# Optimization experiments

Hardware: AMD Instinct MI355X
Metric: run time of the kernel (lower is better)

The kernel has to match this reference:

```python
import jax, jax.numpy as jnp
import numpy as np

B, N, CQ, CH, H = 2, 2048, 256, 256, 8
D = CH // H  # head_dim = 32


def setup_inputs() -> dict:
    key = jax.random.key(0)
    ks = jax.random.split(key, 10)
    s = 0.02
    return {
        "q_x": jax.random.normal(ks[0], (B, N, CQ), dtype=jnp.float32),
        "attn_bias": jax.random.normal(ks[1], (B, H, N, N), dtype=jnp.float32),
        "Wq": jax.random.normal(ks[2], (CQ, CH), dtype=jnp.float32) * s,
        "bq": jnp.zeros((CH,), dtype=jnp.float32),
        "Wk": jax.random.normal(ks[3], (CQ, CH), dtype=jnp.float32) * s,
        "Wv": jax.random.normal(ks[4], (CQ, CH), dtype=jnp.float32) * s,
        "Wout": jax.random.normal(ks[5], (CH, CQ), dtype=jnp.float32) * s,
        "bout": jnp.zeros((CQ,), dtype=jnp.float32),
        "Wg": jax.random.normal(ks[6], (CQ, CQ), dtype=jnp.float32) * s,
        "bg": jnp.zeros((CQ,), dtype=jnp.float32),
        "gbias": jnp.ones((CQ,), dtype=jnp.float32),
    }


def reference(q_x, attn_bias, Wq, bq, Wk, Wv, Wout, bout, Wg, bg, gbias):
    # prep_qkv: project, split heads; scale q by 1/sqrt(head_dim) (apply_scale path)
    scale = 1.0 / jnp.sqrt(jnp.asarray(D, q_x.dtype))
    q = ((q_x @ Wq + bq).reshape(B, N, H, D)) * scale  # [B,N,H,D]
    k = (q_x @ Wk).reshape(B, N, H, D)
    v = (q_x @ Wv).reshape(B, N, H, D)
    # attention with additive pair bias
    scores = jnp.einsum("bqhd,bkhd->bhqk", q, k) + attn_bias  # [B,H,N,N]
    attn = jax.nn.softmax(scores, axis=-1)
    o = jnp.einsum("bhqk,bkhd->bqhd", attn, v).reshape(B, N, CH)  # merge heads
    # wrap_up: output projection + sigmoid gate (gating_bias init ones)
    out = o @ Wout + bout  # [B,N,CQ]
    gate = jax.nn.sigmoid(q_x @ Wg + bg + gbias)
    return gate * out
```

## Files before the change

### kernel.cpp

```cpp
#include <hip/hip_runtime.h>

typedef __bf16 bf16_t;
typedef bf16_t bf16x8 __attribute__((ext_vector_type(8)));
typedef float f32x4 __attribute__((ext_vector_type(4)));
typedef unsigned short ushort8 __attribute__((ext_vector_type(8)));

#define LOG2E 1.4426950408889634f

static __device__ __forceinline__ unsigned short f2bf(float f) {
  union { float f; unsigned u; } a; a.f = f;
  unsigned r = a.u + 0x7FFFu + ((a.u >> 16) & 1u);
  return (unsigned short)(r >> 16);
}

static __device__ __forceinline__ bf16x8 ldb8(const unsigned short* p) {
  return *reinterpret_cast<const bf16x8*>(p);
}

__global__ __launch_bounds__(256) void prep_k(
    const float* __restrict__ Wq, const float* __restrict__ Wk,
    const float* __restrict__ Wv, const float* __restrict__ Wg,
    const float* __restrict__ Wo, const float* __restrict__ X,
    unsigned short* __restrict__ wt, unsigned short* __restrict__ xb) {
  const int bid = blockIdx.x;
  if (bid < 320) {
    __shared__ float t[32][33];
    const int w = bid >> 6, tile = bid & 63;
    const int r0 = (tile >> 3) * 32, c0 = (tile & 7) * 32;
    const float* W = (w == 0) ? Wq : (w == 1) ? Wk : (w == 2) ? Wv : (w == 3) ? Wg : Wo;
    const int x = threadIdx.x & 31, y = threadIdx.x >> 5;
#pragma unroll
    for (int yy = 0; yy < 32; yy += 8) t[y + yy][x] = W[(r0 + y + yy) * 256 + c0 + x];
    __syncthreads();
#pragma unroll
    for (int yy = 0; yy < 32; yy += 8)
      wt[w * 65536 + (c0 + y + yy) * 256 + r0 + x] = f2bf(t[x][y + yy]);
  } else {
    const int i = (bid - 320) * 1024 + threadIdx.x * 4;
    const f32x4 v = *reinterpret_cast<const f32x4*>(X + i);
    unsigned short o[4];
#pragma unroll
    for (int e = 0; e < 4; ++e) o[e] = f2bf(v[e]);
    *reinterpret_cast<unsigned long long*>(xb + i) = *reinterpret_cast<unsigned long long*>(o);
  }
}

__global__ __launch_bounds__(256) void proj_k(
    const unsigned short* __restrict__ xb, const float* __restrict__ bq,
    const unsigned short* __restrict__ wt,
    unsigned short* __restrict__ q_ws, unsigned short* __restrict__ k_ws,
    unsigned short* __restrict__ vt_ws) {
  __shared__ unsigned short vtile[64][72];
  const int tid = threadIdx.x;
  const int wave = tid >> 6, l = tid & 63, g = l >> 4, l15 = l & 15;
  const int mrow = blockIdx.x * 64 + wave * 16 + l15;
  const int widx = blockIdx.y >> 2;
  const int nin0 = (blockIdx.y & 3) * 64;
  const unsigned short* W = wt + widx * 65536;

  f32x4 acc[4];
#pragma unroll
  for (int st = 0; st < 4; ++st) acc[st] = f32x4{0.f, 0.f, 0.f, 0.f};

#pragma unroll
  for (int kk0 = 0; kk0 < 256; kk0 += 32) {
    const bf16x8 av = ldb8(xb + mrow * 256 + kk0 + 8 * g);
#pragma unroll
    for (int st = 0; st < 4; ++st) {
      bf16x8 bv = ldb8(W + (nin0 + st * 16 + l15) * 256 + kk0 + 8 * g);
      acc[st] = __builtin_amdgcn_mfma_f32_16x16x32_bf16(av, bv, acc[st], 0, 0, 0);
    }
  }

  const int mb = blockIdx.x * 64 + wave * 16 + 4 * g;
  if (widx == 2) {
#pragma unroll
    for (int st = 0; st < 4; ++st)
#pragma unroll
      for (int j = 0; j < 4; ++j)
        vtile[st * 16 + l15][wave * 16 + 4 * g + j] = f2bf(acc[st][j]);
    __syncthreads();
    const int b = (blockIdx.x * 64) >> 11;
    const int t0 = (blockIdx.x * 64) & 2047;
#pragma unroll
    for (int it = tid; it < 512; it += 256) {
      const int r = it >> 3, cseg = (it & 7) * 8;
      const int n = nin0 + r;
      *reinterpret_cast<ushort8*>(vt_ws + (size_t)((b * 8 + (n >> 5)) * 32 + (n & 31)) * 2048 +
                                  t0 + cseg) = *reinterpret_cast<const ushort8*>(&vtile[r][cseg]);
    }
  } else {
#pragma unroll
    for (int st = 0; st < 4; ++st) {
      const int n = nin0 + st * 16 + l15;
      const int h = n >> 5, d = n & 31;
#pragma unroll
      for (int j = 0; j < 4; ++j) {
        const int m = mb + j;
        const int b = m >> 11, t = m & 2047;
        if (widx == 0) {
          q_ws[((b * 8 + h) * 2048 + t) * 32 + d] =
              f2bf((acc[st][j] + bq[n]) * (0.17677669529663687f * LOG2E));
        } else {
          k_ws[((b * 8 + h) * 2048 + t) * 32 + d] = f2bf(acc[st][j]);
        }
      }
    }
  }
}

__global__ __launch_bounds__(256) void attn_k(
    const unsigned short* __restrict__ q_ws, const unsigned short* __restrict__ k_ws,
    const unsigned short* __restrict__ vt_ws, const float* __restrict__ bias,
    unsigned short* __restrict__ o_ws) {
  __shared__ float sbias[4 * 3 * 1024];
  __shared__ unsigned short plds[4 * 16 * 72];
  const int tid = threadIdx.x;
  const int wave = tid >> 6, l = tid & 63, g = l >> 4, l15 = l & 15;
  const int bh = blockIdx.x >> 5, qt = blockIdx.x & 31;
  const int qr0 = qt * 64 + wave * 16;
  const int kvbase = bh * 2048;
  unsigned short* pw = plds + wave * (16 * 72);
  float* sb = sbias + wave * 3072;

  const bf16x8 qa = ldb8(q_ws + (size_t)(kvbase + qr0 + l15) * 32 + 8 * g);
  const unsigned short* kbase = k_ws + (size_t)kvbase * 32 + 8 * g + l15 * 32;
  const unsigned short* vbase = vt_ws + (size_t)(bh * 32 + l15) * 2048 + 8 * g;
  const float* bsrc = bias + ((size_t)bh << 22) + (size_t)(qr0 + (l >> 4)) * 2048 + (l & 15) * 4;

  auto stage = [&](int bidx, int k0) {
    float* dst = sb + bidx * 1024;
#pragma unroll
    for (int qq = 0; qq < 4; ++qq)
      __builtin_amdgcn_global_load_lds(
          (const __attribute__((address_space(1))) void*)(bsrc + (size_t)qq * 8192 + k0),
          (__attribute__((address_space(3))) void*)(dst + qq * 256), 16, 0, 0);
  };

  float mr[4], lr[4];
  f32x4 oacc[2];
#pragma unroll
  for (int j = 0; j < 4; ++j) { mr[j] = -1e30f; lr[j] = 0.0f; }
  oacc[0] = f32x4{0.f, 0.f, 0.f, 0.f};
  oacc[1] = f32x4{0.f, 0.f, 0.f, 0.f};

  stage(0, 0);
  stage(1, 64);
  int cb = 0;
#pragma unroll 1
  for (int kt = 0; kt < 32; ++kt) {
    const int k0 = kt * 64;
    if (kt < 31) {
      asm volatile("s_waitcnt vmcnt(4)" ::: "memory");
    } else {
      asm volatile("s_waitcnt vmcnt(0)" ::: "memory");
    }
    __builtin_amdgcn_sched_barrier(0);
    f32x4 cfr[4];
    const float* sbc = sb + cb * 1024 + l15;
#pragma unroll
    for (int st = 0; st < 4; ++st)
#pragma unroll
      for (int j = 0; j < 4; ++j)
        cfr[st][j] = sbc[(4 * g + j) * 64 + st * 16] * LOG2E;

    bf16x8 kb[4];
#pragma unroll
    for (int st = 0; st < 4; ++st) kb[st] = ldb8(kbase + (size_t)(k0 + st * 16) * 32);
    bf16x8 vb[2][2];
#pragma unroll
    for (int dst = 0; dst < 2; ++dst)
#pragma unroll
      for (int kc = 0; kc < 2; ++kc)
        vb[dst][kc] = ldb8(vbase + (size_t)dst * 16 * 2048 + k0 + kc * 32);

    int nb = cb + 2; if (nb >= 3) nb -= 3;
    if (kt < 30) stage(nb, k0 + 128);

    f32x4 s[4];
#pragma unroll
    for (int st = 0; st < 4; ++st)
      s[st] = __builtin_amdgcn_mfma_f32_16x16x32_bf16(qa, kb[st], cfr[st], 0, 0, 0);

#pragma unroll
    for (int j = 0; j < 4; ++j) {
      float mx = fmaxf(fmaxf(s[0][j], s[1][j]), fmaxf(s[2][j], s[3][j]));
      mx = fmaxf(mx, __shfl_xor(mx, 1));
      mx = fmaxf(mx, __shfl_xor(mx, 2));
      mx = fmaxf(mx, __shfl_xor(mx, 4));
      mx = fmaxf(mx, __shfl_xor(mx, 8));
      const float mn = fmaxf(mr[j], mx);
      const float sc = __builtin_amdgcn_exp2f(mr[j] - mn);
      mr[j] = mn;
      float rs = 0.f;
#pragma unroll
      for (int st = 0; st < 4; ++st) {
        float e = __builtin_amdgcn_exp2f(s[st][j] - mn);
        s[st][j] = e;
        rs += e;
      }
      rs += __shfl_xor(rs, 1);
      rs += __shfl_xor(rs, 2);
      rs += __shfl_xor(rs, 4);
      rs += __shfl_xor(rs, 8);
      lr[j] = lr[j] * sc + rs;
      oacc[0][j] *= sc;
      oacc[1][j] *= sc;
    }
#pragma unroll
    for (int st = 0; st < 4; ++st)
#pragma unroll
      for (int j = 0; j < 4; ++j)
        pw[(4 * g + j) * 72 + st * 16 + l15] = f2bf(s[st][j]);
#pragma unroll
    for (int kc = 0; kc < 2; ++kc) {
      bf16x8 pa = ldb8(pw + l15 * 72 + kc * 32 + 8 * g);
      oacc[0] = __builtin_amdgcn_mfma_f32_16x16x32_bf16(pa, vb[0][kc], oacc[0], 0, 0, 0);
      oacc[1] = __builtin_amdgcn_mfma_f32_16x16x32_bf16(pa, vb[1][kc], oacc[1], 0, 0, 0);
    }
    cb = cb + 1; if (cb >= 3) cb -= 3;
  }

  const int b = bh >> 3, h = bh & 7;
#pragma unroll
  for (int dst = 0; dst < 2; ++dst)
#pragma unroll
    for (int j = 0; j < 4; ++j) {
      const int q = qr0 + 4 * g + j;
      const float val = oacc[dst][j] / lr[j];
      o_ws[((size_t)(b * 2048 + q)) * 256 + h * 32 + dst * 16 + l15] = f2bf(val);
    }
}

__global__ __launch_bounds__(256) void outp_k(
    const unsigned short* __restrict__ o_ws, const unsigned short* __restrict__ wt,
    const unsigned short* __restrict__ xb, const float* __restrict__ bout,
    const float* __restrict__ bg, const float* __restrict__ gbias,
    float* __restrict__ out) {
  const int tid = threadIdx.x;
  const int wave = tid >> 6, l = tid & 63, g = l >> 4, l15 = l & 15;
  const int m0 = blockIdx.x * 64 + wave * 16;
  const int c0 = blockIdx.y * 64;
  const unsigned short* wgt = wt + 3 * 65536;
  const unsigned short* wot = wt + 4 * 65536;
  f32x4 acco[4], accg[4];
#pragma unroll
  for (int st = 0; st < 4; ++st) {
    acco[st] = f32x4{0.f, 0.f, 0.f, 0.f};
    accg[st] = f32x4{0.f, 0.f, 0.f, 0.f};
  }
#pragma unroll
  for (int kk0 = 0; kk0 < 256; kk0 += 32) {
    const bf16x8 a_o = ldb8(o_ws + (m0 + l15) * 256 + kk0 + 8 * g);
    const bf16x8 a_x = ldb8(xb + (m0 + l15) * 256 + kk0 + 8 * g);
#pragma unroll
    for (int st = 0; st < 4; ++st) {
      bf16x8 bo = ldb8(wot + (c0 + st * 16 + l15) * 256 + kk0 + 8 * g);
      acco[st] = __builtin_amdgcn_mfma_f32_16x16x32_bf16(a_o, bo, acco[st], 0, 0, 0);
      bf16x8 bgf = ldb8(wgt + (c0 + st * 16 + l15) * 256 + kk0 + 8 * g);
      accg[st] = __builtin_amdgcn_mfma_f32_16x16x32_bf16(a_x, bgf, accg[st], 0, 0, 0);
    }
  }
  const int mb = m0 + 4 * g;
#pragma unroll
  for (int st = 0; st < 4; ++st) {
    const int n = c0 + st * 16 + l15;
#pragma unroll
    for (int j = 0; j < 4; ++j) {
      const int m = mb + j;
      const float z = accg[st][j] + bg[n] + gbias[n];
      const float gate = 1.0f / (1.0f + __expf(-z));
      out[m * 256 + n] = gate * (acco[st][j] + bout[n]);
    }
  }
}

extern "C" void kernel_launch(void* const* d_in, const int* in_sizes, int n_in,
                              void* d_out, int out_size, void* d_ws, size_t ws_size,
                              hipStream_t stream) {
  const float* q_x   = (const float*)d_in[0];
  const float* bias  = (const float*)d_in[1];
  const float* Wq    = (const float*)d_in[2];
  const float* bq    = (const float*)d_in[3];
  const float* Wk    = (const float*)d_in[4];
  const float* Wv    = (const float*)d_in[5];
  const float* Wout  = (const float*)d_in[6];
  const float* bout  = (const float*)d_in[7];
  const float* Wg    = (const float*)d_in[8];
  const float* bg    = (const float*)d_in[9];
  const float* gbias = (const float*)d_in[10];
  float* out = (float*)d_out;

  char* ws = (char*)d_ws;
  unsigned short* wt    = (unsigned short*)(ws);
  unsigned short* xb    = (unsigned short*)(ws + 655360);
  unsigned short* q_ws  = (unsigned short*)(ws + 655360 + 2097152);
  unsigned short* k_ws  = (unsigned short*)(ws + 655360 + 2 * 2097152);
  unsigned short* vt_ws = (unsigned short*)(ws + 655360 + 3 * 2097152);
  unsigned short* o_ws  = (unsigned short*)(ws + 655360 + 4 * 2097152);

  prep_k<<<1344, 256, 0, stream>>>(Wq, Wk, Wv, Wg, Wout, q_x, wt, xb);
  proj_k<<<dim3(64, 12), 256, 0, stream>>>(xb, bq, wt, q_ws, k_ws, vt_ws);
  attn_k<<<512, 256, 0, stream>>>(q_ws, k_ws, vt_ws, bias, o_ws);
  outp_k<<<dim3(64, 4), 256, 0, stream>>>(o_ws, wt, xb, bout, bg, gbias, out);
}
```

Baseline: 112.0 us.

## Double-buffer 128-key bias tiles and issue K/V loads before bias wait

The attention kernel now stages the pair bias in 128-key tiles with two LDS buffers per wave, replacing three 64-key buffers. Each loop iteration handles two 64-key halves, which halves the number of iterations and the loop overhead. K and V fragments for both halves are loaded before the wait on the next bias tile, so their latency overlaps with it. The cost is more registers for K/V fragments, a larger LDS footprint (64KB of bias), and hand-tuned vmcnt counts that depend on the exact order of the loads.

```diff
diff --git a/kernel.cpp b/kernel.cpp
--- a/kernel.cpp
+++ b/kernel.cpp
@@ -113,28 +113,27 @@
     const unsigned short* __restrict__ q_ws, const unsigned short* __restrict__ k_ws,
     const unsigned short* __restrict__ vt_ws, const float* __restrict__ bias,
     unsigned short* __restrict__ o_ws) {
-  __shared__ float sbias[4 * 3 * 1024];
-  __shared__ unsigned short plds[4 * 16 * 72];
+  __shared__ float sbias[4][2][16][128];
+  __shared__ unsigned short plds[4][16 * 72];
   const int tid = threadIdx.x;
   const int wave = tid >> 6, l = tid & 63, g = l >> 4, l15 = l & 15;
   const int bh = blockIdx.x >> 5, qt = blockIdx.x & 31;
   const int qr0 = qt * 64 + wave * 16;
   const int kvbase = bh * 2048;
-  unsigned short* pw = plds + wave * (16 * 72);
-  float* sb = sbias + wave * 3072;
+  unsigned short* pw = plds[wave];
 
   const bf16x8 qa = ldb8(q_ws + (size_t)(kvbase + qr0 + l15) * 32 + 8 * g);
   const unsigned short* kbase = k_ws + (size_t)kvbase * 32 + 8 * g + l15 * 32;
   const unsigned short* vbase = vt_ws + (size_t)(bh * 32 + l15) * 2048 + 8 * g;
-  const float* bsrc = bias + ((size_t)bh << 22) + (size_t)(qr0 + (l >> 4)) * 2048 + (l & 15) * 4;
-
-  auto stage = [&](int bidx, int k0) {
-    float* dst = sb + bidx * 1024;
-#pragma unroll
-    for (int qq = 0; qq < 4; ++qq)
+  const float* bsrc = bias + ((size_t)bh << 22) + (size_t)(qr0 + (l >> 5)) * 2048 + (l & 31) * 4;
+
+  auto stage = [&](int buf, int kt) {
+    float* dst = &sbias[wave][buf][0][0];
+#pragma unroll
+    for (int i = 0; i < 8; ++i)
       __builtin_amdgcn_global_load_lds(
-          (const __attribute__((address_space(1))) void*)(bsrc + (size_t)qq * 8192 + k0),
-          (__attribute__((address_space(3))) void*)(dst + qq * 256), 16, 0, 0);
+          (const __attribute__((address_space(1))) void*)(bsrc + (size_t)(2 * i) * 2048 + kt * 128),
+          (__attribute__((address_space(3))) void*)(dst + i * 256), 16, 0, 0);
   };
 
   float mr[4], lr[4];
@@ -145,80 +144,81 @@
   oacc[1] = f32x4{0.f, 0.f, 0.f, 0.f};
 
   stage(0, 0);
-  stage(1, 64);
-  int cb = 0;
 #pragma unroll 1
-  for (int kt = 0; kt < 32; ++kt) {
-    const int k0 = kt * 64;
-    if (kt < 31) {
-      asm volatile("s_waitcnt vmcnt(4)" ::: "memory");
+  for (int kt = 0; kt < 16; ++kt) {
+    const int buf = kt & 1;
+    const int k0 = kt * 128;
+    bf16x8 kb[2][4];
+#pragma unroll
+    for (int h = 0; h < 2; ++h)
+#pragma unroll
+      for (int st = 0; st < 4; ++st)
+        kb[h][st] = ldb8(kbase + (size_t)(k0 + h * 64 + st * 16) * 32);
+    bf16x8 vb[2][2][2];
+#pragma unroll
+    for (int h = 0; h < 2; ++h)
+#pragma unroll
+      for (int dst = 0; dst < 2; ++dst)
+#pragma unroll
+        for (int kc = 0; kc < 2; ++kc)
+          vb[h][dst][kc] = ldb8(vbase + (size_t)dst * 16 * 2048 + k0 + h * 64 + kc * 32);
+    if (kt < 15) stage(buf ^ 1, kt + 1);
+    if (kt < 15) {
+      asm volatile("s_waitcnt vmcnt(24)" ::: "memory");
     } else {
-      asm volatile("s_waitcnt vmcnt(0)" ::: "memory");
+      asm volatile("s_waitcnt vmcnt(16)" ::: "memory");
     }
     __builtin_amdgcn_sched_barrier(0);
-    f32x4 cfr[4];
-    const float* sbc = sb + cb * 1024 + l15;
-#pragma unroll
-    for (int st = 0; st < 4; ++st)
-#pragma unroll
-      for (int j = 0; j < 4; ++j)
-        cfr[st][j] = sbc[(4 * g + j) * 64 + st * 16] * LOG2E;
-
-    bf16x8 kb[4];
-#pragma unroll
-    for (int st = 0; st < 4; ++st) kb[st] = ldb8(kbase + (size_t)(k0 + st * 16) * 32);
-    bf16x8 vb[2][2];
-#pragma unroll
-    for (int dst = 0; dst < 2; ++dst)
-#pragma unroll
-      for (int kc = 0; kc < 2; ++kc)
-        vb[dst][kc] = ldb8(vbase + (size_t)dst * 16 * 2048 + k0 + kc * 32);
-
-    int nb = cb + 2; if (nb >= 3) nb -= 3;
-    if (kt < 30) stage(nb, k0 + 128);
-
-    f32x4 s[4];
-#pragma unroll
-    for (int st = 0; st < 4; ++st)
-      s[st] = __builtin_amdgcn_mfma_f32_16x16x32_bf16(qa, kb[st], cfr[st], 0, 0, 0);
-
-#pragma unroll
-    for (int j = 0; j < 4; ++j) {
-      float mx = fmaxf(fmaxf(s[0][j], s[1][j]), fmaxf(s[2][j], s[3][j]));
-      mx = fmaxf(mx, __shfl_xor(mx, 1));
-      mx = fmaxf(mx, __shfl_xor(mx, 2));
-      mx = fmaxf(mx, __shfl_xor(mx, 4));
-      mx = fmaxf(mx, __shfl_xor(mx, 8));
-      const float mn = fmaxf(mr[j], mx);
-      const float sc = __builtin_amdgcn_exp2f(mr[j] - mn);
-      mr[j] = mn;
-      float rs = 0.f;
-#pragma unroll
-      for (int st = 0; st < 4; ++st) {
-        float e = __builtin_amdgcn_exp2f(s[st][j] - mn);
-        s[st][j] = e;
-        rs += e;
+
+#pragma unroll
+    for (int h = 0; h < 2; ++h) {
+      f32x4 cfr[4];
+#pragma unroll
+      for (int st = 0; st < 4; ++st)
+#pragma unroll
+        for (int j = 0; j < 4; ++j)
+          cfr[st][j] = sbias[wave][buf][4 * g + j][h * 64 + st * 16 + l15] * LOG2E;
+      f32x4 s[4];
+#pragma unroll
+      for (int st = 0; st < 4; ++st)
+        s[st] = __builtin_amdgcn_mfma_f32_16x16x32_bf16(qa, kb[h][st], cfr[st], 0, 0, 0);
+#pragma unroll
+      for (int j = 0; j < 4; ++j) {
+        float mx = fmaxf(fmaxf(s[0][j], s[1][j]), fmaxf(s[2][j], s[3][j]));
+        mx = fmaxf(mx, __shfl_xor(mx, 1));
+        mx = fmaxf(mx, __shfl_xor(mx, 2));
+        mx = fmaxf(mx, __shfl_xor(mx, 4));
+        mx = fmaxf(mx, __shfl_xor(mx, 8));
+        const float mn = fmaxf(mr[j], mx);
+        const float sc = __builtin_amdgcn_exp2f(mr[j] - mn);
+        mr[j] = mn;
+        float rs = 0.f;
+#pragma unroll
+        for (int st = 0; st < 4; ++st) {
+          float e = __builtin_amdgcn_exp2f(s[st][j] - mn);
+          s[st][j] = e;
+          rs += e;
+        }
+        rs += __shfl_xor(rs, 1);
+        rs += __shfl_xor(rs, 2);
+        rs += __shfl_xor(rs, 4);
+        rs += __shfl_xor(rs, 8);
+        lr[j] = lr[j] * sc + rs;
+        oacc[0][j] *= sc;
+        oacc[1][j] *= sc;
       }
-      rs += __shfl_xor(rs, 1);
-      rs += __shfl_xor(rs, 2);
-      rs += __shfl_xor(rs, 4);
-      rs += __shfl_xor(rs, 8);
-      lr[j] = lr[j] * sc + rs;
-      oacc[0][j] *= sc;
-      oacc[1][j] *= sc;
-    }
-#pragma unroll
-    for (int st = 0; st < 4; ++st)
-#pragma unroll
-      for (int j = 0; j < 4; ++j)
-        pw[(4 * g + j) * 72 + st * 16 + l15] = f2bf(s[st][j]);
-#pragma unroll
-    for (int kc = 0; kc < 2; ++kc) {
-      bf16x8 pa = ldb8(pw + l15 * 72 + kc * 32 + 8 * g);
-      oacc[0] = __builtin_amdgcn_mfma_f32_16x16x32_bf16(pa, vb[0][kc], oacc[0], 0, 0, 0);
-      oacc[1] = __builtin_amdgcn_mfma_f32_16x16x32_bf16(pa, vb[1][kc], oacc[1], 0, 0, 0);
-    }
-    cb = cb + 1; if (cb >= 3) cb -= 3;
+#pragma unroll
+      for (int st = 0; st < 4; ++st)
+#pragma unroll
+        for (int j = 0; j < 4; ++j)
+          pw[(4 * g + j) * 72 + st * 16 + l15] = f2bf(s[st][j]);
+#pragma unroll
+      for (int kc = 0; kc < 2; ++kc) {
+        bf16x8 pa = ldb8(pw + l15 * 72 + kc * 32 + 8 * g);
+        oacc[0] = __builtin_amdgcn_mfma_f32_16x16x32_bf16(pa, vb[h][0][kc], oacc[0], 0, 0, 0);
+        oacc[1] = __builtin_amdgcn_mfma_f32_16x16x32_bf16(pa, vb[h][1][kc], oacc[1], 0, 0, 0);
+      }
+    }
   }
 
   const int b = bh >> 3, h = bh & 7;
```

Measured after the change: 121.9 us. 8.9% more time.

## Fuse bf16 conversion into projection kernels and double-buffer bias staging

Applied to the files above, without the earlier changes.

Removes the separate prep kernel. The projection and output kernels now read fp32 inputs and weights directly, converting weights to bf16 and transposing them into shared memory, and converting activations to bf16 in registers. This drops one launch and a workspace round trip. In exchange, every block redoes the weight conversion, and the weight loads are strided column reads. The attention kernel also moves from triple- to double-buffered bias staging with a full vmcnt(0) wait and a launch-bounds occupancy hint, trading prefetch depth for less LDS per block.

```diff
diff --git a/kernel.cpp b/kernel.cpp
--- a/kernel.cpp
+++ b/kernel.cpp
@@ -17,46 +17,28 @@
   return *reinterpret_cast<const bf16x8*>(p);
 }
 
-__global__ __launch_bounds__(256) void prep_k(
+__global__ __launch_bounds__(256) void proj_k(
+    const float* __restrict__ X, const float* __restrict__ bq,
     const float* __restrict__ Wq, const float* __restrict__ Wk,
-    const float* __restrict__ Wv, const float* __restrict__ Wg,
-    const float* __restrict__ Wo, const float* __restrict__ X,
-    unsigned short* __restrict__ wt, unsigned short* __restrict__ xb) {
-  const int bid = blockIdx.x;
-  if (bid < 320) {
-    __shared__ float t[32][33];
-    const int w = bid >> 6, tile = bid & 63;
-    const int r0 = (tile >> 3) * 32, c0 = (tile & 7) * 32;
-    const float* W = (w == 0) ? Wq : (w == 1) ? Wk : (w == 2) ? Wv : (w == 3) ? Wg : Wo;
-    const int x = threadIdx.x & 31, y = threadIdx.x >> 5;
-#pragma unroll
-    for (int yy = 0; yy < 32; yy += 8) t[y + yy][x] = W[(r0 + y + yy) * 256 + c0 + x];
-    __syncthreads();
-#pragma unroll
-    for (int yy = 0; yy < 32; yy += 8)
-      wt[w * 65536 + (c0 + y + yy) * 256 + r0 + x] = f2bf(t[x][y + yy]);
-  } else {
-    const int i = (bid - 320) * 1024 + threadIdx.x * 4;
-    const f32x4 v = *reinterpret_cast<const f32x4*>(X + i);
-    unsigned short o[4];
-#pragma unroll
-    for (int e = 0; e < 4; ++e) o[e] = f2bf(v[e]);
-    *reinterpret_cast<unsigned long long*>(xb + i) = *reinterpret_cast<unsigned long long*>(o);
-  }
-}
-
-__global__ __launch_bounds__(256) void proj_k(
-    const unsigned short* __restrict__ xb, const float* __restrict__ bq,
-    const unsigned short* __restrict__ wt,
+    const float* __restrict__ Wv,
     unsigned short* __restrict__ q_ws, unsigned short* __restrict__ k_ws,
     unsigned short* __restrict__ vt_ws) {
+  __shared__ unsigned short wl[64][264];
   __shared__ unsigned short vtile[64][72];
   const int tid = threadIdx.x;
   const int wave = tid >> 6, l = tid & 63, g = l >> 4, l15 = l & 15;
   const int mrow = blockIdx.x * 64 + wave * 16 + l15;
   const int widx = blockIdx.y >> 2;
   const int nin0 = (blockIdx.y & 3) * 64;
-  const unsigned short* W = wt + widx * 65536;
+  const float* W = (widx == 0) ? Wq : (widx == 1) ? Wk : Wv;
+
+  {
+    const int c = tid & 63;
+#pragma unroll
+    for (int kk = tid >> 6; kk < 256; kk += 4)
+      wl[c][kk] = f2bf(W[kk * 256 + nin0 + c]);
+  }
+  __syncthreads();
 
   f32x4 acc[4];
 #pragma unroll
@@ -64,11 +46,16 @@
 
 #pragma unroll
   for (int kk0 = 0; kk0 < 256; kk0 += 32) {
-    const bf16x8 av = ldb8(xb + mrow * 256 + kk0 + 8 * g);
+    const float* xp = X + mrow * 256 + kk0 + 8 * g;
+    f32x4 x0 = *reinterpret_cast<const f32x4*>(xp);
+    f32x4 x1 = *reinterpret_cast<const f32x4*>(xp + 4);
+    union { unsigned short u[8]; bf16x8 v; } av;
+#pragma unroll
+    for (int e = 0; e < 4; ++e) { av.u[e] = f2bf(x0[e]); av.u[4 + e] = f2bf(x1[e]); }
 #pragma unroll
     for (int st = 0; st < 4; ++st) {
-      bf16x8 bv = ldb8(W + (nin0 + st * 16 + l15) * 256 + kk0 + 8 * g);
-      acc[st] = __builtin_amdgcn_mfma_f32_16x16x32_bf16(av, bv, acc[st], 0, 0, 0);
+      bf16x8 bv = ldb8(&wl[st * 16 + l15][kk0 + 8 * g]);
+      acc[st] = __builtin_amdgcn_mfma_f32_16x16x32_bf16(av.v, bv, acc[st], 0, 0, 0);
     }
   }
 
@@ -109,27 +96,26 @@
   }
 }
 
-__global__ __launch_bounds__(256) void attn_k(
+__global__ __launch_bounds__(256, 3) void attn_k(
     const unsigned short* __restrict__ q_ws, const unsigned short* __restrict__ k_ws,
     const unsigned short* __restrict__ vt_ws, const float* __restrict__ bias,
     unsigned short* __restrict__ o_ws) {
-  __shared__ float sbias[4 * 3 * 1024];
-  __shared__ unsigned short plds[4 * 16 * 72];
+  __shared__ float sbias[4][2][1024];
+  __shared__ unsigned short plds[4][16 * 72];
   const int tid = threadIdx.x;
   const int wave = tid >> 6, l = tid & 63, g = l >> 4, l15 = l & 15;
   const int bh = blockIdx.x >> 5, qt = blockIdx.x & 31;
   const int qr0 = qt * 64 + wave * 16;
   const int kvbase = bh * 2048;
-  unsigned short* pw = plds + wave * (16 * 72);
-  float* sb = sbias + wave * 3072;
+  unsigned short* pw = plds[wave];
 
   const bf16x8 qa = ldb8(q_ws + (size_t)(kvbase + qr0 + l15) * 32 + 8 * g);
   const unsigned short* kbase = k_ws + (size_t)kvbase * 32 + 8 * g + l15 * 32;
   const unsigned short* vbase = vt_ws + (size_t)(bh * 32 + l15) * 2048 + 8 * g;
   const float* bsrc = bias + ((size_t)bh << 22) + (size_t)(qr0 + (l >> 4)) * 2048 + (l & 15) * 4;
 
-  auto stage = [&](int bidx, int k0) {
-    float* dst = sb + bidx * 1024;
+  auto stage = [&](int buf, int k0) {
+    float* dst = &sbias[wave][buf][0];
 #pragma unroll
     for (int qq = 0; qq < 4; ++qq)
       __builtin_amdgcn_global_load_lds(
@@ -145,19 +131,14 @@
   oacc[1] = f32x4{0.f, 0.f, 0.f, 0.f};
 
   stage(0, 0);
-  stage(1, 64);
-  int cb = 0;
 #pragma unroll 1
   for (int kt = 0; kt < 32; ++kt) {
+    const int buf = kt & 1;
     const int k0 = kt * 64;
-    if (kt < 31) {
-      asm volatile("s_waitcnt vmcnt(4)" ::: "memory");
-    } else {
-      asm volatile("s_waitcnt vmcnt(0)" ::: "memory");
-    }
+    asm volatile("s_waitcnt vmcnt(0)" ::: "memory");
     __builtin_amdgcn_sched_barrier(0);
     f32x4 cfr[4];
-    const float* sbc = sb + cb * 1024 + l15;
+    const float* sbc = &sbias[wave][buf][0] + l15;
 #pragma unroll
     for (int st = 0; st < 4; ++st)
 #pragma unroll
@@ -174,8 +155,7 @@
       for (int kc = 0; kc < 2; ++kc)
         vb[dst][kc] = ldb8(vbase + (size_t)dst * 16 * 2048 + k0 + kc * 32);
 
-    int nb = cb + 2; if (nb >= 3) nb -= 3;
-    if (kt < 30) stage(nb, k0 + 128);
+    if (kt < 31) stage(buf ^ 1, k0 + 64);
 
     f32x4 s[4];
 #pragma unroll
@@ -218,7 +198,6 @@
       oacc[0] = __builtin_amdgcn_mfma_f32_16x16x32_bf16(pa, vb[0][kc], oacc[0], 0, 0, 0);
       oacc[1] = __builtin_amdgcn_mfma_f32_16x16x32_bf16(pa, vb[1][kc], oacc[1], 0, 0, 0);
     }
-    cb = cb + 1; if (cb >= 3) cb -= 3;
   }
 
   const int b = bh >> 3, h = bh & 7;
@@ -233,16 +212,27 @@
 }
 
 __global__ __launch_bounds__(256) void outp_k(
-    const unsigned short* __restrict__ o_ws, const unsigned short* __restrict__ wt,
-    const unsigned short* __restrict__ xb, const float* __restrict__ bout,
-    const float* __restrict__ bg, const float* __restrict__ gbias,
-    float* __restrict__ out) {
+    const unsigned short* __restrict__ o_ws, const float* __restrict__ X,
+    const float* __restrict__ Wg, const float* __restrict__ Wo,
+    const float* __restrict__ bout, const float* __restrict__ bg,
+    const float* __restrict__ gbias, float* __restrict__ out) {
+  __shared__ unsigned short wgl[64][264];
+  __shared__ unsigned short wol[64][264];
   const int tid = threadIdx.x;
   const int wave = tid >> 6, l = tid & 63, g = l >> 4, l15 = l & 15;
   const int m0 = blockIdx.x * 64 + wave * 16;
   const int c0 = blockIdx.y * 64;
-  const unsigned short* wgt = wt + 3 * 65536;
-  const unsigned short* wot = wt + 4 * 65536;
+
+  {
+    const int c = tid & 63;
+#pragma unroll
+    for (int kk = tid >> 6; kk < 256; kk += 4) {
+      wgl[c][kk] = f2bf(Wg[kk * 256 + c0 + c]);
+      wol[c][kk] = f2bf(Wo[kk * 256 + c0 + c]);
+    }
+  }
+  __syncthreads();
+
   f32x4 acco[4], accg[4];
 #pragma unroll
   for (int st = 0; st < 4; ++st) {
@@ -252,13 +242,18 @@
 #pragma unroll
   for (int kk0 = 0; kk0 < 256; kk0 += 32) {
     const bf16x8 a_o = ldb8(o_ws + (m0 + l15) * 256 + kk0 + 8 * g);
-    const bf16x8 a_x = ldb8(xb + (m0 + l15) * 256 + kk0 + 8 * g);
+    const float* xp = X + (m0 + l15) * 256 + kk0 + 8 * g;
+    f32x4 x0 = *reinterpret_cast<const f32x4*>(xp);
+    f32x4 x1 = *reinterpret_cast<const f32x4*>(xp + 4);
+    union { unsigned short u[8]; bf16x8 v; } av;
+#pragma unroll
+    for (int e = 0; e < 4; ++e) { av.u[e] = f2bf(x0[e]); av.u[4 + e] = f2bf(x1[e]); }
 #pragma unroll
     for (int st = 0; st < 4; ++st) {
-      bf16x8 bo = ldb8(wot + (c0 + st * 16 + l15) * 256 + kk0 + 8 * g);
+      bf16x8 bo = ldb8(&wol[st * 16 + l15][kk0 + 8 * g]);
       acco[st] = __builtin_amdgcn_mfma_f32_16x16x32_bf16(a_o, bo, acco[st], 0, 0, 0);
-      bf16x8 bgf = ldb8(wgt + (c0 + st * 16 + l15) * 256 + kk0 + 8 * g);
-      accg[st] = __builtin_amdgcn_mfma_f32_16x16x32_bf16(a_x, bgf, accg[st], 0, 0, 0);
+      bf16x8 bgf = ldb8(&wgl[st * 16 + l15][kk0 + 8 * g]);
+      accg[st] = __builtin_amdgcn_mfma_f32_16x16x32_bf16(av.v, bgf, accg[st], 0, 0, 0);
     }
   }
   const int mb = m0 + 4 * g;
@@ -292,15 +287,12 @@
   float* out = (float*)d_out;
 
   char* ws = (char*)d_ws;
-  unsigned short* wt    = (unsigned short*)(ws);
-  unsigned short* xb    = (unsigned short*)(ws + 655360);
-  unsigned short* q_ws  = (unsigned short*)(ws + 655360 + 2097152);
-  unsigned short* k_ws  = (unsigned short*)(ws + 655360 + 2 * 2097152);
-  unsigned short* vt_ws = (unsigned short*)(ws + 655360 + 3 * 2097152);
-  unsigned short* o_ws  = (unsigned short*)(ws + 655360 + 4 * 2097152);
-
-  prep_k<<<1344, 256, 0, stream>>>(Wq, Wk, Wv, Wg, Wout, q_x, wt, xb);
-  proj_k<<<dim3(64, 12), 256, 0, stream>>>(xb, bq, wt, q_ws, k_ws, vt_ws);
+  unsigned short* q_ws  = (unsigned short*)(ws);
+  unsigned short* k_ws  = (unsigned short*)(ws + 2097152);
+  unsigned short* vt_ws = (unsigned short*)(ws + 2 * 2097152);
+  unsigned short* o_ws  = (unsigned short*)(ws + 3 * 2097152);
+
+  proj_k<<<dim3(64, 12), 256, 0, stream>>>(q_x, bq, Wq, Wk, Wv, q_ws, k_ws, vt_ws);
   attn_k<<<512, 256, 0, stream>>>(q_ws, k_ws, vt_ws, bias, o_ws);
-  outp_k<<<dim3(64, 4), 256, 0, stream>>>(o_ws, wt, xb, bout, bg, gbias, out);
-}
+  outp_k<<<dim3(64, 4), 256, 0, stream>>>(o_ws, q_x, Wg, Wout, bout, bg, gbias, out);
+}
```

Measured after the change: 95.33 us. 14.9% less time.
